# Performance work log

Measured on AMD Instinct MI355X. Metric: run time of the kernel, lower is better.

The kernel has to match this reference:

```python
import jax, jax.numpy as jnp
import numpy as np

B, S, D = 2, 2048, 1024
H, HD = 16, 64  # n_heads, head_dim


def setup_inputs() -> dict:
    key = jax.random.key(0)
    ks = jax.random.split(key, 6)
    scale = 1.0 / np.sqrt(D)
    return {
        "Q": jax.random.normal(ks[0], (B, S, D), dtype=jnp.float32),
        "K": jax.random.normal(ks[1], (B, S, D), dtype=jnp.float32),
        "V": jax.random.normal(ks[2], (B, S, D), dtype=jnp.float32),
        "Wq": jax.random.normal(ks[3], (H, D, HD), dtype=jnp.float32) * scale,
        "Wv": jax.random.normal(ks[4], (H, D, HD), dtype=jnp.float32) * scale,
        "Wo": jax.random.normal(ks[5], (D, D), dtype=jnp.float32) * scale,
        "bo": jnp.zeros((D,), dtype=jnp.float32),
    }


def reference(Q, K, V, Wq, Wv, Wo, bo):
    # NOTE: original code projects K with the *query* weight (bug kept for fidelity).
    q = jnp.einsum("bsd,hdk->bhsk", Q, Wq)   # [B,H,S,HD]
    k = jnp.einsum("bsd,hdk->bhsk", K, Wq)   # query weights, per original
    v = jnp.einsum("bsd,hdk->bhsk", V, Wv)
    scores = jnp.einsum("bhsk,bhtk->bhst", q, k) / jnp.sqrt(jnp.asarray(HD, q.dtype))
    weights = jax.nn.softmax(scores, axis=-1)  # [B,H,S,S]
    attn = jnp.einsum("bhst,bhtk->bhsk", weights, v)  # [B,H,S,HD]
    concat = attn.transpose(0, 2, 1, 3).reshape(Q.shape[0], Q.shape[1], H * HD)
    return concat @ Wo.T + bo
```

## Files before the change

### kernel.cpp

```cpp
#include <hip/hip_runtime.h>

typedef __attribute__((ext_vector_type(8))) short short8;
typedef __attribute__((ext_vector_type(4))) short short4v;
typedef __attribute__((ext_vector_type(4))) float f32x4;

__device__ __forceinline__ unsigned short f2bf(float f) {
  union { float f; unsigned u; } v; v.f = f;
  unsigned u = v.u;
  unsigned r = (u + 0x7FFFu + ((u >> 16) & 1u)) >> 16;
  return (unsigned short)r;
}

__device__ __forceinline__ unsigned cvtpk(float lo, float hi) {
  unsigned r;
  asm("v_cvt_pk_bf16_f32 %0, %1, %2" : "=v"(r) : "v"(lo), "v"(hi));
  return r;
}

#if __has_builtin(__builtin_amdgcn_exp2f)
__device__ __forceinline__ float exp2_fast(float x) { return __builtin_amdgcn_exp2f(x); }
#else
__device__ __forceinline__ float exp2_fast(float x) { return __expf(x * 0.69314718056f); }
#endif

__device__ __forceinline__ void gl16(const void* g, void* l) {
  __builtin_amdgcn_global_load_lds(
      (const __attribute__((address_space(1))) unsigned int*)g,
      (__attribute__((address_space(3))) unsigned int*)l, 16, 0, 0);
}

#define QSCALE 0.1803368801111f

__global__ __launch_bounds__(256)
void prep_k(const float* __restrict__ Wq, const float* __restrict__ Wv,
            const float* __restrict__ Wo, unsigned short* __restrict__ BqT,
            unsigned short* __restrict__ BvT, unsigned short* __restrict__ BoT) {
  __shared__ float tile[64 * 65];
  const int bidx = blockIdx.x;
  const int tid = threadIdx.x;
  if (bidx < 512) {
    const float* W = (bidx < 256) ? Wq : Wv;
    unsigned short* Bt = (bidx < 256) ? BqT : BvT;
    const int bb = bidx & 255;
    const int h  = bb >> 4;
    const int d0 = (bb & 15) * 64;
#pragma unroll
    for (int i = 0; i < 16; ++i) {
      int e = i * 256 + tid;
      int r = e >> 6, c = e & 63;
      tile[r * 65 + c] = W[(size_t)h * 65536 + (size_t)(d0 + r) * 64 + c];
    }
    __syncthreads();
#pragma unroll
    for (int i = 0; i < 16; ++i) {
      int e = i * 256 + tid;
      int jj = e >> 6, dd = e & 63;
      Bt[(size_t)(h * 64 + jj) * 1024 + d0 + dd] = f2bf(tile[dd * 65 + jj]);
    }
  } else {
    size_t t = (size_t)(bidx - 512) * 256 + tid;
    float4 f = *(const float4*)(Wo + t * 4);
    short4v v;
    v[0] = (short)f2bf(f.x); v[1] = (short)f2bf(f.y);
    v[2] = (short)f2bf(f.z); v[3] = (short)f2bf(f.w);
    *(short4v*)((short*)BoT + t * 4) = v;
  }
}

__global__ __launch_bounds__(256)
void conv3_k(const float* __restrict__ Q, const float* __restrict__ K,
             const float* __restrict__ V, unsigned short* __restrict__ dst) {
  const int bidx = blockIdx.x;
  const int sec = bidx >> 11;
  const float* src = (sec == 0) ? Q : (sec == 1) ? K : V;
  const float scale = (sec == 0) ? QSCALE : 1.0f;
  size_t t = (size_t)(bidx & 2047) * 256 + threadIdx.x;
  const float* s = src + t * 8;
  float4 f0 = *(const float4*)s;
  float4 f1 = *(const float4*)(s + 4);
  short8 v;
  v[0] = (short)f2bf(f0.x * scale); v[1] = (short)f2bf(f0.y * scale);
  v[2] = (short)f2bf(f0.z * scale); v[3] = (short)f2bf(f0.w * scale);
  v[4] = (short)f2bf(f1.x * scale); v[5] = (short)f2bf(f1.y * scale);
  v[6] = (short)f2bf(f1.z * scale); v[7] = (short)f2bf(f1.w * scale);
  *(short8*)(dst + (size_t)sec * 4194304 + t * 8) = v;
}

__global__ __launch_bounds__(256)
void vtrans_k(const unsigned short* __restrict__ vh, unsigned short* __restrict__ vT) {
  __shared__ unsigned short tile[64][72];
  const int st = blockIdx.x & 31;
  const int h = (blockIdx.x >> 5) & 15;
  const int b = blockIdx.x >> 9;
  const int t = threadIdx.x;
  const int r0 = t >> 3, c0 = (t & 7) * 8;
#pragma unroll
  for (int i = 0; i < 2; ++i) {
    int r = r0 + i * 32;
    short8 v = *(const short8*)(vh + (size_t)(b * 2048 + st * 64 + r) * 1024 + h * 64 + c0);
    *(short8*)&tile[r][c0] = v;
  }
  __syncthreads();
#pragma unroll
  for (int i = 0; i < 2; ++i) {
    int hd = r0 + i * 32;
    short8 v;
#pragma unroll
    for (int j = 0; j < 8; ++j) v[j] = tile[c0 + j][hd];
    *(short8*)(vT + (size_t)((b * 16 + h) * 64 + hd) * 2048 + st * 64 + c0) = v;
  }
}

template<int EPI>
__global__ __launch_bounds__(256, 2)
void gemm3_k(const unsigned short* __restrict__ A, const unsigned short* __restrict__ Bt,
             void* __restrict__ Cp, const float* __restrict__ bias) {
  __shared__ __attribute__((aligned(16))) unsigned short As[2][64 * 64];
  __shared__ __attribute__((aligned(16))) unsigned short Bs[2][128 * 64];
  const int tid = threadIdx.x;
  const int l = tid & 63;
  const int w = tid >> 6;
  const int wr = w >> 1, wc = w & 1;
  const int lg = l >> 4, lc = l & 15;
  const int nwg = (int)gridDim.x;
  const int bid = blockIdx.x;
  const int swz = (bid & 7) * (nwg >> 3) + (bid >> 3);
  const int bm = swz >> 3, bn = swz & 7;

  const int sr = tid >> 3, ss = tid & 7;
  const unsigned short* Asrc = A  + (size_t)(bm * 64  + sr) * 1024 + ((ss ^ (sr & 7)) * 8);
  const unsigned short* Bsrc = Bt + (size_t)(bn * 128 + sr) * 1024 + ((ss ^ (sr & 7)) * 8);

  f32x4 acc[2][4] = {};

  auto stage = [&](int bufn, int k0) {
    char* ad = (char*)&As[bufn][0] + tid * 16;
    char* bd = (char*)&Bs[bufn][0] + tid * 16;
    gl16(Asrc + k0,          ad);
    gl16(Asrc + 32768 + k0,  ad + 4096);
    gl16(Bsrc + k0,          bd);
    gl16(Bsrc + 32768 + k0,  bd + 4096);
    gl16(Bsrc + 65536 + k0,  bd + 8192);
    gl16(Bsrc + 98304 + k0,  bd + 12288);
  };

  stage(0, 0);
  __syncthreads();

  int buf = 0;
  for (int it = 0; it < 16; ++it) {
    if (it < 15) stage(buf ^ 1, (it + 1) * 64);
    const unsigned short* Ac = &As[buf][0];
    const unsigned short* Bc = &Bs[buf][0];
    short8 af[2][2], bf[4][2];
#pragma unroll
    for (int mi = 0; mi < 2; ++mi)
#pragma unroll
      for (int ks = 0; ks < 2; ++ks)
        af[mi][ks] = *(const short8*)&Ac[(wr * 32 + mi * 16 + lc) * 64 + (((ks * 4 + lg) ^ (lc & 7)) * 8)];
#pragma unroll
    for (int ni = 0; ni < 4; ++ni)
#pragma unroll
      for (int ks = 0; ks < 2; ++ks)
        bf[ni][ks] = *(const short8*)&Bc[(wc * 64 + ni * 16 + lc) * 64 + (((ks * 4 + lg) ^ (lc & 7)) * 8)];
#pragma unroll
    for (int mi = 0; mi < 2; ++mi)
#pragma unroll
      for (int ni = 0; ni < 4; ++ni) {
        acc[mi][ni] = __builtin_amdgcn_mfma_f32_16x16x32_bf16(af[mi][0], bf[ni][0], acc[mi][ni], 0, 0, 0);
        acc[mi][ni] = __builtin_amdgcn_mfma_f32_16x16x32_bf16(af[mi][1], bf[ni][1], acc[mi][ni], 0, 0, 0);
      }
    __syncthreads();
    buf ^= 1;
  }

  const int m0 = bm * 64 + wr * 32 + lg * 4;
  const int n0 = bn * 128 + wc * 64 + lc;
#pragma unroll
  for (int mi = 0; mi < 2; ++mi) {
#pragma unroll
    for (int ni = 0; ni < 4; ++ni) {
#pragma unroll
      for (int j = 0; j < 4; ++j) {
        int m = m0 + mi * 16 + j;
        int n = n0 + ni * 16;
        if (EPI == 2) ((float*)Cp)[(size_t)m * 1024 + n] = acc[mi][ni][j] + bias[n];
        else          ((unsigned short*)Cp)[(size_t)m * 1024 + n] = f2bf(acc[mi][ni][j]);
      }
    }
  }
}

__global__ __launch_bounds__(256, 3)
void attn_k(const unsigned short* __restrict__ qh, const unsigned short* __restrict__ kh,
            const unsigned short* __restrict__ vT, unsigned short* __restrict__ attnc) {
  __shared__ __attribute__((aligned(16))) short Kb[2][4096];
  __shared__ __attribute__((aligned(16))) short Vb[2][4096];
  __shared__ __attribute__((aligned(16))) short Pl[4][2][1152];

  const int bid = (blockIdx.x & 7) * 64 + (blockIdx.x >> 3);
  const int qt = bid & 15;
  const int h = (bid >> 4) & 15;
  const int b = bid >> 8;
  const int tid = threadIdx.x;
  const int l = tid & 63;
  const int w = tid >> 6;
  const int lg = l >> 4;
  const int lc = l & 15;

  const unsigned short* qb  = qh + (size_t)(b * 2048) * 1024 + h * 64;
  const unsigned short* kbf = kh + (size_t)(b * 2048) * 1024 + h * 64;
  const unsigned short* vb  = vT + (size_t)((b * 16 + h) * 64) * 2048;

  const int sr = tid >> 3, ss = tid & 7;
  const unsigned short* Ksrc = kbf + (size_t)sr * 1024 + ((ss ^ (sr & 7)) * 8);
  const unsigned short* Vsrc = vb  + (size_t)sr * 2048 + ((ss ^ (sr & 7)) * 8);

  const int s0 = qt * 128 + w * 16;
  const short8 qA0 = *(const short8*)(qb + (size_t)(s0 + lc) * 1024 + lg * 8);
  const short8 qA1 = *(const short8*)(qb + (size_t)(s0 + lc) * 1024 + 32 + lg * 8);
  const short8 qB0 = *(const short8*)(qb + (size_t)(s0 + 64 + lc) * 1024 + lg * 8);
  const short8 qB1 = *(const short8*)(qb + (size_t)(s0 + 64 + lc) * 1024 + 32 + lg * 8);

  const int go = (lg ^ (lc & 7)) * 8;

  float mA = -1e30f, lA = 0.f, mB = -1e30f, lB = 0.f;
  f32x4 accA[4] = {}, accB[4] = {};
  short* pwA = &Pl[w][0][0];
  short* pwB = &Pl[w][1][0];
  const f32x4 zero = {0.f, 0.f, 0.f, 0.f};

  auto stageKV = [&](int bufn, int t0) {
    char* kd = (char*)&Kb[bufn][0] + tid * 16;
    char* vd = (char*)&Vb[bufn][0] + tid * 16;
    const unsigned short* ks = Ksrc + (size_t)t0 * 1024;
    const unsigned short* vs = Vsrc + t0;
    gl16(ks,         kd);
    gl16(ks + 32768, kd + 4096);
    gl16(vs,         vd);
    gl16(vs + 65536, vd + 4096);
  };

  stageKV(0, 0);
  __syncthreads();

  int cur = 0;
  for (int i = 0; i < 32; ++i) {
    if (i < 31) stageKV(cur ^ 1, (i + 1) * 64);

    const short* Kc = &Kb[cur][0];
    f32x4 sA[4], sB[4];
#pragma unroll
    for (int kk = 0; kk < 4; ++kk) {
      const short* krow = Kc + (kk * 16 + lc) * 64;
      short8 k0 = *(const short8*)(krow + go);
      short8 k1 = *(const short8*)(krow + (go ^ 32));
      sA[kk] = __builtin_amdgcn_mfma_f32_16x16x32_bf16(k0, qA0, zero, 0, 0, 0);
      sA[kk] = __builtin_amdgcn_mfma_f32_16x16x32_bf16(k1, qA1, sA[kk], 0, 0, 0);
      sB[kk] = __builtin_amdgcn_mfma_f32_16x16x32_bf16(k0, qB0, zero, 0, 0, 0);
      sB[kk] = __builtin_amdgcn_mfma_f32_16x16x32_bf16(k1, qB1, sB[kk], 0, 0, 0);
    }

    float tA = fmaxf(fmaxf(fmaxf(sA[0][0], sA[0][1]), fmaxf(sA[0][2], sA[0][3])),
                     fmaxf(fmaxf(sA[1][0], sA[1][1]), fmaxf(sA[1][2], sA[1][3])));
    tA = fmaxf(tA, fmaxf(fmaxf(fmaxf(sA[2][0], sA[2][1]), fmaxf(sA[2][2], sA[2][3])),
                         fmaxf(fmaxf(sA[3][0], sA[3][1]), fmaxf(sA[3][2], sA[3][3]))));
    float tB = fmaxf(fmaxf(fmaxf(sB[0][0], sB[0][1]), fmaxf(sB[0][2], sB[0][3])),
                     fmaxf(fmaxf(sB[1][0], sB[1][1]), fmaxf(sB[1][2], sB[1][3])));
    tB = fmaxf(tB, fmaxf(fmaxf(fmaxf(sB[2][0], sB[2][1]), fmaxf(sB[2][2], sB[2][3])),
                         fmaxf(fmaxf(sB[3][0], sB[3][1]), fmaxf(sB[3][2], sB[3][3]))));

    if (!__all(fmaxf(tA - mA, tB - mB) <= 8.0f)) {
      tA = fmaxf(tA, __shfl_xor(tA, 16)); tA = fmaxf(tA, __shfl_xor(tA, 32));
      tB = fmaxf(tB, __shfl_xor(tB, 16)); tB = fmaxf(tB, __shfl_xor(tB, 32));
      float mnA = fmaxf(mA, tA), mnB = fmaxf(mB, tB);
      float scA = exp2_fast(mA - mnA), scB = exp2_fast(mB - mnB);
      mA = mnA; mB = mnB; lA *= scA; lB *= scB;
      float sAj[4], sBj[4];
#pragma unroll
      for (int j = 0; j < 4; ++j) {
        sAj[j] = __shfl(scA, lg * 4 + j);
        sBj[j] = __shfl(scB, lg * 4 + j);
      }
#pragma unroll
      for (int n = 0; n < 4; ++n)
#pragma unroll
        for (int j = 0; j < 4; ++j) { accA[n][j] *= sAj[j]; accB[n][j] *= sBj[j]; }
    }

#pragma unroll
    for (int kk = 0; kk < 4; ++kk) {
      float p0 = exp2_fast(sA[kk][0] - mA), p1 = exp2_fast(sA[kk][1] - mA);
      float p2 = exp2_fast(sA[kk][2] - mA), p3 = exp2_fast(sA[kk][3] - mA);
      lA += (p0 + p1) + (p2 + p3);
      uint2 pk; pk.x = cvtpk(p0, p1); pk.y = cvtpk(p2, p3);
      *(uint2*)((char*)pwA + lc * 144 + kk * 32 + lg * 8) = pk;
      float q0 = exp2_fast(sB[kk][0] - mB), q1 = exp2_fast(sB[kk][1] - mB);
      float q2 = exp2_fast(sB[kk][2] - mB), q3 = exp2_fast(sB[kk][3] - mB);
      lB += (q0 + q1) + (q2 + q3);
      uint2 qk2; qk2.x = cvtpk(q0, q1); qk2.y = cvtpk(q2, q3);
      *(uint2*)((char*)pwB + lc * 144 + kk * 32 + lg * 8) = qk2;
    }

    short8 pA0 = *(const short8*)&pwA[lc * 72 + lg * 8];
    short8 pA1 = *(const short8*)&pwA[lc * 72 + 32 + lg * 8];
    short8 pB0 = *(const short8*)&pwB[lc * 72 + lg * 8];
    short8 pB1 = *(const short8*)&pwB[lc * 72 + 32 + lg * 8];

    const short* Vc = &Vb[cur][0];
#pragma unroll
    for (int n = 0; n < 4; ++n) {
      const short* vrow = Vc + (n * 16 + lc) * 64;
      short8 v0 = *(const short8*)(vrow + go);
      short8 v1 = *(const short8*)(vrow + (go ^ 32));
      accA[n] = __builtin_amdgcn_mfma_f32_16x16x32_bf16(pA0, v0, accA[n], 0, 0, 0);
      accA[n] = __builtin_amdgcn_mfma_f32_16x16x32_bf16(pA1, v1, accA[n], 0, 0, 0);
      accB[n] = __builtin_amdgcn_mfma_f32_16x16x32_bf16(pB0, v0, accB[n], 0, 0, 0);
      accB[n] = __builtin_amdgcn_mfma_f32_16x16x32_bf16(pB1, v1, accB[n], 0, 0, 0);
    }

    __syncthreads();
    cur ^= 1;
  }

  lA += __shfl_xor(lA, 16); lA += __shfl_xor(lA, 32);
  lB += __shfl_xor(lB, 16); lB += __shfl_xor(lB, 32);
  float invA = 1.0f / lA, invB = 1.0f / lB;
  float iAj[4], iBj[4];
#pragma unroll
  for (int j = 0; j < 4; ++j) {
    iAj[j] = __shfl(invA, lg * 4 + j);
    iBj[j] = __shfl(invB, lg * 4 + j);
  }
#pragma unroll
  for (int n = 0; n < 4; ++n)
#pragma unroll
    for (int j = 0; j < 4; ++j) {
      int col = h * 64 + n * 16 + lc;
      int sA_ = s0 + lg * 4 + j;
      attnc[(size_t)(b * 2048 + sA_) * 1024 + col]      = f2bf(accA[n][j] * iAj[j]);
      attnc[(size_t)(b * 2048 + sA_ + 64) * 1024 + col] = f2bf(accB[n][j] * iBj[j]);
    }
}

extern "C" void kernel_launch(void* const* d_in, const int* in_sizes, int n_in,
                              void* d_out, int out_size, void* d_ws, size_t ws_size,
                              hipStream_t stream) {
  const float* Q  = (const float*)d_in[0];
  const float* Kt = (const float*)d_in[1];
  const float* V  = (const float*)d_in[2];
  const float* Wq = (const float*)d_in[3];
  const float* Wv = (const float*)d_in[4];
  const float* Wo = (const float*)d_in[5];
  const float* bo = (const float*)d_in[6];
  float* out = (float*)d_out;

  char* ws = (char*)d_ws;
  unsigned short* QKb  = (unsigned short*)(ws);
  unsigned short* Vb   = (unsigned short*)(ws + ((size_t)16 << 20));
  unsigned short* qh   = (unsigned short*)(ws + ((size_t)24 << 20));
  unsigned short* BqT  = (unsigned short*)(ws + ((size_t)40 << 20));
  unsigned short* BvT  = (unsigned short*)(ws + ((size_t)42 << 20));
  unsigned short* BoT  = (unsigned short*)(ws + ((size_t)44 << 20));
  unsigned short* vh   = QKb;
  unsigned short* vT   = (unsigned short*)(ws + ((size_t)8 << 20));
  unsigned short* attc = Vb;
  unsigned short* kh   = qh + (size_t)4096 * 1024;

  prep_k<<<1536, 256, 0, stream>>>(Wq, Wv, Wo, BqT, BvT, BoT);
  conv3_k<<<6144, 256, 0, stream>>>(Q, Kt, V, QKb);

  gemm3_k<0><<<1024, 256, 0, stream>>>(QKb, BqT, qh, nullptr);
  gemm3_k<0><<<512, 256, 0, stream>>>(Vb, BvT, vh, nullptr);

  vtrans_k<<<1024, 256, 0, stream>>>(vh, vT);

  attn_k<<<512, 256, 0, stream>>>(qh, kh, vT, attc);

  gemm3_k<2><<<512, 256, 0, stream>>>(attc, BoT, out, bo);
}
```

Baseline: 146.1 us.

## Fuse V transpose into projection epilogue and use 32x32 MFMA attention

The V projection GEMM now writes its output directly in the transposed per-head layout through a new epilogue, so the separate transpose kernel and its extra round trip through global memory go away. The attention kernel moves from 16x16x32 to 32x32x16 MFMA tiles, with each wave owning 32 query rows. Probabilities are repacked into the B operand with cross-lane shuffles instead of a shared-memory staging buffer, and the output is written with vectorized stores. The epilogue's transposed stores are narrow 8-byte strided writes, and the occupancy hint drops from 3 to 2 blocks per CU to give the larger accumulators room.

```diff
diff --git a/kernel.cpp b/kernel.cpp
--- a/kernel.cpp
+++ b/kernel.cpp
@@ -3,6 +3,7 @@
 typedef __attribute__((ext_vector_type(8))) short short8;
 typedef __attribute__((ext_vector_type(4))) short short4v;
 typedef __attribute__((ext_vector_type(4))) float f32x4;
+typedef __attribute__((ext_vector_type(16))) float f32x16;
 
 __device__ __forceinline__ unsigned short f2bf(float f) {
   union { float f; unsigned u; } v; v.f = f;
@@ -86,31 +87,6 @@
   *(short8*)(dst + (size_t)sec * 4194304 + t * 8) = v;
 }
 
-__global__ __launch_bounds__(256)
-void vtrans_k(const unsigned short* __restrict__ vh, unsigned short* __restrict__ vT) {
-  __shared__ unsigned short tile[64][72];
-  const int st = blockIdx.x & 31;
-  const int h = (blockIdx.x >> 5) & 15;
-  const int b = blockIdx.x >> 9;
-  const int t = threadIdx.x;
-  const int r0 = t >> 3, c0 = (t & 7) * 8;
-#pragma unroll
-  for (int i = 0; i < 2; ++i) {
-    int r = r0 + i * 32;
-    short8 v = *(const short8*)(vh + (size_t)(b * 2048 + st * 64 + r) * 1024 + h * 64 + c0);
-    *(short8*)&tile[r][c0] = v;
-  }
-  __syncthreads();
-#pragma unroll
-  for (int i = 0; i < 2; ++i) {
-    int hd = r0 + i * 32;
-    short8 v;
-#pragma unroll
-    for (int j = 0; j < 8; ++j) v[j] = tile[c0 + j][hd];
-    *(short8*)(vT + (size_t)((b * 16 + h) * 64 + hd) * 2048 + st * 64 + c0) = v;
-  }
-}
-
 template<int EPI>
 __global__ __launch_bounds__(256, 2)
 void gemm3_k(const unsigned short* __restrict__ A, const unsigned short* __restrict__ Bt,
@@ -180,23 +156,50 @@
   for (int mi = 0; mi < 2; ++mi) {
 #pragma unroll
     for (int ni = 0; ni < 4; ++ni) {
-#pragma unroll
-      for (int j = 0; j < 4; ++j) {
-        int m = m0 + mi * 16 + j;
+      if (EPI == 1) {
+        int m = m0 + mi * 16;
+        int bb = m >> 11, s = m & 2047;
         int n = n0 + ni * 16;
-        if (EPI == 2) ((float*)Cp)[(size_t)m * 1024 + n] = acc[mi][ni][j] + bias[n];
-        else          ((unsigned short*)Cp)[(size_t)m * 1024 + n] = f2bf(acc[mi][ni][j]);
+        int hh = n >> 6, hd = n & 63;
+        short4v pk;
+#pragma unroll
+        for (int j = 0; j < 4; ++j) pk[j] = (short)f2bf(acc[mi][ni][j]);
+        *(short4v*)((unsigned short*)Cp + (size_t)((bb * 16 + hh) * 64 + hd) * 2048 + s) = pk;
+      } else {
+#pragma unroll
+        for (int j = 0; j < 4; ++j) {
+          int m = m0 + mi * 16 + j;
+          int n = n0 + ni * 16;
+          if (EPI == 2) ((float*)Cp)[(size_t)m * 1024 + n] = acc[mi][ni][j] + bias[n];
+          else          ((unsigned short*)Cp)[(size_t)m * 1024 + n] = f2bf(acc[mi][ni][j]);
+        }
       }
     }
   }
 }
 
-__global__ __launch_bounds__(256, 3)
+#define PACK8(SV, B0, W)                                                   \
+  {                                                                        \
+    float e0 = exp2_fast(SV[B0 + 0] - m_r), e1 = exp2_fast(SV[B0 + 1] - m_r); \
+    float e2 = exp2_fast(SV[B0 + 2] - m_r), e3 = exp2_fast(SV[B0 + 3] - m_r); \
+    float e4 = exp2_fast(SV[B0 + 4] - m_r), e5 = exp2_fast(SV[B0 + 5] - m_r); \
+    float e6 = exp2_fast(SV[B0 + 6] - m_r), e7 = exp2_fast(SV[B0 + 7] - m_r); \
+    l_r += ((e0 + e1) + (e2 + e3)) + ((e4 + e5) + (e6 + e7));              \
+    unsigned Wa = cvtpk(e0, e1), Wb = cvtpk(e2, e3);                       \
+    unsigned Wc = cvtpk(e4, e5), Wd = cvtpk(e6, e7);                       \
+    unsigned pWa = __shfl_xor((int)Wa, 32), pWb = __shfl_xor((int)Wb, 32); \
+    unsigned pWc = __shfl_xor((int)Wc, 32), pWd = __shfl_xor((int)Wd, 32); \
+    W.x = hi ? pWc : Wa; W.y = hi ? pWd : Wb;                              \
+    W.z = hi ? Wc : pWa; W.w = hi ? Wd : pWb;                              \
+  }
+
+#define MAX4(V, I) fmaxf(fmaxf(V[I], V[I + 1]), fmaxf(V[I + 2], V[I + 3]))
+
+__global__ __launch_bounds__(256, 2)
 void attn_k(const unsigned short* __restrict__ qh, const unsigned short* __restrict__ kh,
             const unsigned short* __restrict__ vT, unsigned short* __restrict__ attnc) {
   __shared__ __attribute__((aligned(16))) short Kb[2][4096];
   __shared__ __attribute__((aligned(16))) short Vb[2][4096];
-  __shared__ __attribute__((aligned(16))) short Pl[4][2][1152];
 
   const int bid = (blockIdx.x & 7) * 64 + (blockIdx.x >> 3);
   const int qt = bid & 15;
@@ -205,8 +208,9 @@
   const int tid = threadIdx.x;
   const int l = tid & 63;
   const int w = tid >> 6;
-  const int lg = l >> 4;
-  const int lc = l & 15;
+  const int q = l & 31;
+  const int hi = l >> 5;
+  const int ax = l & 7;
 
   const unsigned short* qb  = qh + (size_t)(b * 2048) * 1024 + h * 64;
   const unsigned short* kbf = kh + (size_t)(b * 2048) * 1024 + h * 64;
@@ -216,19 +220,15 @@
   const unsigned short* Ksrc = kbf + (size_t)sr * 1024 + ((ss ^ (sr & 7)) * 8);
   const unsigned short* Vsrc = vb  + (size_t)sr * 2048 + ((ss ^ (sr & 7)) * 8);
 
-  const int s0 = qt * 128 + w * 16;
-  const short8 qA0 = *(const short8*)(qb + (size_t)(s0 + lc) * 1024 + lg * 8);
-  const short8 qA1 = *(const short8*)(qb + (size_t)(s0 + lc) * 1024 + 32 + lg * 8);
-  const short8 qB0 = *(const short8*)(qb + (size_t)(s0 + 64 + lc) * 1024 + lg * 8);
-  const short8 qB1 = *(const short8*)(qb + (size_t)(s0 + 64 + lc) * 1024 + 32 + lg * 8);
-
-  const int go = (lg ^ (lc & 7)) * 8;
-
-  float mA = -1e30f, lA = 0.f, mB = -1e30f, lB = 0.f;
-  f32x4 accA[4] = {}, accB[4] = {};
-  short* pwA = &Pl[w][0][0];
-  short* pwB = &Pl[w][1][0];
-  const f32x4 zero = {0.f, 0.f, 0.f, 0.f};
+  const int s0 = qt * 128 + w * 32;
+  short8 qf[4];
+#pragma unroll
+  for (int c = 0; c < 4; ++c)
+    qf[c] = *(const short8*)(qb + (size_t)(s0 + q) * 1024 + c * 16 + hi * 8);
+
+  float m_r = -1e30f, l_r = 0.f;
+  f32x16 acc0 = {}, acc1 = {};
+  const f32x16 zero16 = {};
 
   auto stageKV = [&](int bufn, int t0) {
     char* kd = (char*)&Kb[bufn][0] + tid * 16;
@@ -249,98 +249,70 @@
     if (i < 31) stageKV(cur ^ 1, (i + 1) * 64);
 
     const short* Kc = &Kb[cur][0];
-    f32x4 sA[4], sB[4];
-#pragma unroll
-    for (int kk = 0; kk < 4; ++kk) {
-      const short* krow = Kc + (kk * 16 + lc) * 64;
-      short8 k0 = *(const short8*)(krow + go);
-      short8 k1 = *(const short8*)(krow + (go ^ 32));
-      sA[kk] = __builtin_amdgcn_mfma_f32_16x16x32_bf16(k0, qA0, zero, 0, 0, 0);
-      sA[kk] = __builtin_amdgcn_mfma_f32_16x16x32_bf16(k1, qA1, sA[kk], 0, 0, 0);
-      sB[kk] = __builtin_amdgcn_mfma_f32_16x16x32_bf16(k0, qB0, zero, 0, 0, 0);
-      sB[kk] = __builtin_amdgcn_mfma_f32_16x16x32_bf16(k1, qB1, sB[kk], 0, 0, 0);
-    }
-
-    float tA = fmaxf(fmaxf(fmaxf(sA[0][0], sA[0][1]), fmaxf(sA[0][2], sA[0][3])),
-                     fmaxf(fmaxf(sA[1][0], sA[1][1]), fmaxf(sA[1][2], sA[1][3])));
-    tA = fmaxf(tA, fmaxf(fmaxf(fmaxf(sA[2][0], sA[2][1]), fmaxf(sA[2][2], sA[2][3])),
-                         fmaxf(fmaxf(sA[3][0], sA[3][1]), fmaxf(sA[3][2], sA[3][3]))));
-    float tB = fmaxf(fmaxf(fmaxf(sB[0][0], sB[0][1]), fmaxf(sB[0][2], sB[0][3])),
-                     fmaxf(fmaxf(sB[1][0], sB[1][1]), fmaxf(sB[1][2], sB[1][3])));
-    tB = fmaxf(tB, fmaxf(fmaxf(fmaxf(sB[2][0], sB[2][1]), fmaxf(sB[2][2], sB[2][3])),
-                         fmaxf(fmaxf(sB[3][0], sB[3][1]), fmaxf(sB[3][2], sB[3][3]))));
-
-    if (!__all(fmaxf(tA - mA, tB - mB) <= 8.0f)) {
-      tA = fmaxf(tA, __shfl_xor(tA, 16)); tA = fmaxf(tA, __shfl_xor(tA, 32));
-      tB = fmaxf(tB, __shfl_xor(tB, 16)); tB = fmaxf(tB, __shfl_xor(tB, 32));
-      float mnA = fmaxf(mA, tA), mnB = fmaxf(mB, tB);
-      float scA = exp2_fast(mA - mnA), scB = exp2_fast(mB - mnB);
-      mA = mnA; mB = mnB; lA *= scA; lB *= scB;
-      float sAj[4], sBj[4];
-#pragma unroll
-      for (int j = 0; j < 4; ++j) {
-        sAj[j] = __shfl(scA, lg * 4 + j);
-        sBj[j] = __shfl(scB, lg * 4 + j);
-      }
-#pragma unroll
-      for (int n = 0; n < 4; ++n)
-#pragma unroll
-        for (int j = 0; j < 4; ++j) { accA[n][j] *= sAj[j]; accB[n][j] *= sBj[j]; }
-    }
-
-#pragma unroll
-    for (int kk = 0; kk < 4; ++kk) {
-      float p0 = exp2_fast(sA[kk][0] - mA), p1 = exp2_fast(sA[kk][1] - mA);
-      float p2 = exp2_fast(sA[kk][2] - mA), p3 = exp2_fast(sA[kk][3] - mA);
-      lA += (p0 + p1) + (p2 + p3);
-      uint2 pk; pk.x = cvtpk(p0, p1); pk.y = cvtpk(p2, p3);
-      *(uint2*)((char*)pwA + lc * 144 + kk * 32 + lg * 8) = pk;
-      float q0 = exp2_fast(sB[kk][0] - mB), q1 = exp2_fast(sB[kk][1] - mB);
-      float q2 = exp2_fast(sB[kk][2] - mB), q3 = exp2_fast(sB[kk][3] - mB);
-      lB += (q0 + q1) + (q2 + q3);
-      uint2 qk2; qk2.x = cvtpk(q0, q1); qk2.y = cvtpk(q2, q3);
-      *(uint2*)((char*)pwB + lc * 144 + kk * 32 + lg * 8) = qk2;
-    }
-
-    short8 pA0 = *(const short8*)&pwA[lc * 72 + lg * 8];
-    short8 pA1 = *(const short8*)&pwA[lc * 72 + 32 + lg * 8];
-    short8 pB0 = *(const short8*)&pwB[lc * 72 + lg * 8];
-    short8 pB1 = *(const short8*)&pwB[lc * 72 + 32 + lg * 8];
+    f32x16 sv0 = zero16, sv1 = zero16;
+#pragma unroll
+    for (int c = 0; c < 4; ++c) {
+      const int gofs = (((c * 2 + hi) ^ ax) * 8);
+      short8 kf0 = *(const short8*)&Kc[(q) * 64 + gofs];
+      short8 kf1 = *(const short8*)&Kc[(32 + q) * 64 + gofs];
+      sv0 = __builtin_amdgcn_mfma_f32_32x32x16_bf16(kf0, qf[c], sv0, 0, 0, 0);
+      sv1 = __builtin_amdgcn_mfma_f32_32x32x16_bf16(kf1, qf[c], sv1, 0, 0, 0);
+    }
+
+    float tA = fmaxf(fmaxf(MAX4(sv0, 0), MAX4(sv0, 4)), fmaxf(MAX4(sv0, 8), MAX4(sv0, 12)));
+    float tB = fmaxf(fmaxf(MAX4(sv1, 0), MAX4(sv1, 4)), fmaxf(MAX4(sv1, 8), MAX4(sv1, 12)));
+    float tm = fmaxf(tA, tB);
+
+    if (!__all(tm - m_r <= 8.0f)) {
+      tm = fmaxf(tm, __shfl_xor(tm, 32));
+      float mn = fmaxf(m_r, tm);
+      float sc = exp2_fast(m_r - mn);
+      m_r = mn;
+      l_r *= sc;
+#pragma unroll
+      for (int j = 0; j < 16; ++j) { acc0[j] *= sc; acc1[j] *= sc; }
+    }
+
+    uint4 w0, w1, w2, w3;
+    PACK8(sv0, 0, w0);
+    PACK8(sv0, 8, w1);
+    PACK8(sv1, 0, w2);
+    PACK8(sv1, 8, w3);
+    short8 pf0 = *reinterpret_cast<short8*>(&w0);
+    short8 pf1 = *reinterpret_cast<short8*>(&w1);
+    short8 pf2 = *reinterpret_cast<short8*>(&w2);
+    short8 pf3 = *reinterpret_cast<short8*>(&w3);
 
     const short* Vc = &Vb[cur][0];
 #pragma unroll
-    for (int n = 0; n < 4; ++n) {
-      const short* vrow = Vc + (n * 16 + lc) * 64;
-      short8 v0 = *(const short8*)(vrow + go);
-      short8 v1 = *(const short8*)(vrow + (go ^ 32));
-      accA[n] = __builtin_amdgcn_mfma_f32_16x16x32_bf16(pA0, v0, accA[n], 0, 0, 0);
-      accA[n] = __builtin_amdgcn_mfma_f32_16x16x32_bf16(pA1, v1, accA[n], 0, 0, 0);
-      accB[n] = __builtin_amdgcn_mfma_f32_16x16x32_bf16(pB0, v0, accB[n], 0, 0, 0);
-      accB[n] = __builtin_amdgcn_mfma_f32_16x16x32_bf16(pB1, v1, accB[n], 0, 0, 0);
+    for (int kc = 0; kc < 4; ++kc) {
+      const int gofs = (((kc * 2 + hi) ^ ax) * 8);
+      short8 vf0 = *(const short8*)&Vc[(q) * 64 + gofs];
+      short8 vf1 = *(const short8*)&Vc[(32 + q) * 64 + gofs];
+      short8 pf = (kc == 0) ? pf0 : (kc == 1) ? pf1 : (kc == 2) ? pf2 : pf3;
+      acc0 = __builtin_amdgcn_mfma_f32_32x32x16_bf16(vf0, pf, acc0, 0, 0, 0);
+      acc1 = __builtin_amdgcn_mfma_f32_32x32x16_bf16(vf1, pf, acc1, 0, 0, 0);
     }
 
     __syncthreads();
     cur ^= 1;
   }
 
-  lA += __shfl_xor(lA, 16); lA += __shfl_xor(lA, 32);
-  lB += __shfl_xor(lB, 16); lB += __shfl_xor(lB, 32);
-  float invA = 1.0f / lA, invB = 1.0f / lB;
-  float iAj[4], iBj[4];
-#pragma unroll
-  for (int j = 0; j < 4; ++j) {
-    iAj[j] = __shfl(invA, lg * 4 + j);
-    iBj[j] = __shfl(invB, lg * 4 + j);
-  }
-#pragma unroll
-  for (int n = 0; n < 4; ++n)
-#pragma unroll
-    for (int j = 0; j < 4; ++j) {
-      int col = h * 64 + n * 16 + lc;
-      int sA_ = s0 + lg * 4 + j;
-      attnc[(size_t)(b * 2048 + sA_) * 1024 + col]      = f2bf(accA[n][j] * iAj[j]);
-      attnc[(size_t)(b * 2048 + sA_ + 64) * 1024 + col] = f2bf(accB[n][j] * iBj[j]);
-    }
+  l_r += __shfl_xor(l_r, 32);
+  float inv = 1.0f / l_r;
+
+  unsigned short* outp = attnc + (size_t)(b * 2048 + s0 + q) * 1024 + h * 64;
+#pragma unroll
+  for (int t = 0; t < 4; ++t) {
+    short4v p0, p1;
+#pragma unroll
+    for (int n = 0; n < 4; ++n) {
+      p0[n] = (short)f2bf(acc0[t * 4 + n] * inv);
+      p1[n] = (short)f2bf(acc1[t * 4 + n] * inv);
+    }
+    *(short4v*)(outp + (t * 8 + 4 * hi))      = p0;
+    *(short4v*)(outp + (32 + t * 8 + 4 * hi)) = p1;
+  }
 }
 
 extern "C" void kernel_launch(void* const* d_in, const int* in_sizes, int n_in,
@@ -362,18 +334,15 @@
   unsigned short* BqT  = (unsigned short*)(ws + ((size_t)40 << 20));
   unsigned short* BvT  = (unsigned short*)(ws + ((size_t)42 << 20));
   unsigned short* BoT  = (unsigned short*)(ws + ((size_t)44 << 20));
-  unsigned short* vh   = QKb;
-  unsigned short* vT   = (unsigned short*)(ws + ((size_t)8 << 20));
-  unsigned short* attc = Vb;
+  unsigned short* vT   = QKb;
+  unsigned short* attc = (unsigned short*)(ws + ((size_t)8 << 20));
   unsigned short* kh   = qh + (size_t)4096 * 1024;
 
   prep_k<<<1536, 256, 0, stream>>>(Wq, Wv, Wo, BqT, BvT, BoT);
   conv3_k<<<6144, 256, 0, stream>>>(Q, Kt, V, QKb);
 
   gemm3_k<0><<<1024, 256, 0, stream>>>(QKb, BqT, qh, nullptr);
-  gemm3_k<0><<<512, 256, 0, stream>>>(Vb, BvT, vh, nullptr);
-
-  vtrans_k<<<1024, 256, 0, stream>>>(vh, vT);
+  gemm3_k<1><<<512, 256, 0, stream>>>(Vb, BvT, vT, nullptr);
 
   attn_k<<<512, 256, 0, stream>>>(qh, kh, vT, attc);
 
```

Measured after the change: 142.0 us. 2.8% less time.
